# Optimization experiments

Measured on AMD Instinct MI355X. Metric: run time of the kernel, lower is better.

Reference implementation:

```python
import jax, jax.numpy as jnp
import numpy as np

C = 0.1          # curvature
EPS = 1e-8
BN_EPS = 1e-5
MAX_NORM = 0.9

def batchnorm_train(x, gamma, beta):
    mu = jnp.mean(x, axis=0)
    var = jnp.var(x, axis=0)  # biased, matches torch BN normalization
    return gamma * (x - mu) * jax.lax.rsqrt(var + BN_EPS) + beta

def euclidean_to_poincare(x, c=C, max_norm=MAX_NORM):
    norm = jnp.linalg.norm(x, axis=-1, keepdims=True)
    zeros_mask = norm == 0
    safe_norm = jnp.where(zeros_mask, jnp.ones_like(norm), norm)
    sqrt_c = jnp.sqrt(jnp.asarray(c, x.dtype))
    scale = max_norm * jnp.tanh(sqrt_c * norm) / (sqrt_c * safe_norm)
    return jnp.where(zeros_mask, jnp.zeros_like(x), scale * x)

def poincare_to_euclidean(x, c=C):
    norms = jnp.linalg.norm(x, axis=-1, keepdims=True)
    norms = jnp.clip(norms, 1e-8, 1.0 - 1e-8)
    sqrt_c = jnp.sqrt(jnp.asarray(c, x.dtype))
    return x * jnp.arctanh(sqrt_c * norms) / (sqrt_c * norms)

def batch_poincare_exp_map(x, v, c=C):
    x_nsq = jnp.sum(x * x, axis=-1, keepdims=True)
    lambda_x = 2.0 / (1.0 - c * x_nsq + EPS)
    v_norm = jnp.linalg.norm(v, axis=-1, keepdims=True)
    v_norm = jnp.maximum(v_norm, EPS)
    sqrt_c = jnp.sqrt(jnp.asarray(c, x.dtype))
    scale = jnp.tanh(sqrt_c * lambda_x * v_norm / 2.0) / (sqrt_c * v_norm)
    sv = scale * v
    numerator = (1.0 - c * x_nsq) * sv
    x_sv = jnp.sum(x * sv, axis=-1, keepdims=True)
    sv_nsq = jnp.sum(sv * sv, axis=-1, keepdims=True)
    denom = 1.0 - 2.0 * c * x_sv + c * c * x_nsq * sv_nsq
    result = x + numerator / (denom + EPS)
    mask = jnp.all(jnp.isfinite(result), axis=-1, keepdims=True)
    return jnp.where(mask, result, jnp.zeros_like(result))

def batch_poincare_log_map(x, y, c=C):
    x_nsq = jnp.sum(x * x, axis=-1, keepdims=True)
    lambda_x = 2.0 / (1.0 - c * x_nsq + EPS)
    y_nsq = jnp.sum(y * y, axis=-1, keepdims=True)
    xy = jnp.sum(x * y, axis=-1, keepdims=True)
    numerator = (1.0 - 2.0 * c * xy + c * y_nsq) * x - (1.0 - c * x_nsq) * y
    denom = 1.0 - 2.0 * c * xy + c * c * x_nsq * y_nsq
    diff = numerator / (denom + EPS)
    diff_norm = jnp.linalg.norm(diff, axis=-1, keepdims=True)
    diff_norm = jnp.maximum(diff_norm, EPS)
    sqrt_c = jnp.sqrt(jnp.asarray(c, x.dtype))
    return 2.0 / (sqrt_c * lambda_x) * jnp.arctanh(sqrt_c * diff_norm) * diff / diff_norm

def setup_inputs() -> dict:
    key = jax.random.key(0)
    ks = jax.random.split(key, 8)
    B, D_IN, H, D_OUT = 8192, 1024, 2048, 1000
    x = jax.random.normal(ks[0], (B, D_IN), dtype=jnp.float32)
    # kaiming_normal fan_out: std = sqrt(2/fan_out) with fan_out = out_features
    W1 = jax.random.normal(ks[1], (H, D_IN), dtype=jnp.float32) * np.sqrt(2.0 / H)
    b1 = jnp.zeros((H,), jnp.float32)
    g1 = jnp.ones((H,), jnp.float32)
    be1 = jnp.zeros((H,), jnp.float32)
    W2 = jax.random.normal(ks[2], (H, H), dtype=jnp.float32) * np.sqrt(2.0 / H)
    b2 = jnp.zeros((H,), jnp.float32)
    g2 = jnp.ones((H,), jnp.float32)
    be2 = jnp.zeros((H,), jnp.float32)
    W3 = jax.random.normal(ks[3], (D_OUT, H), dtype=jnp.float32) * np.sqrt(2.0 / D_OUT)
    b3 = jnp.zeros((D_OUT,), jnp.float32)
    return {"x": x, "W1": W1, "b1": b1, "g1": g1, "be1": be1,
            "W2": W2, "b2": b2, "g2": g2, "be2": be2, "W3": W3, "b3": b3}

def reference(x, W1, b1, g1, be1, W2, b2, g2, be2, W3, b3):
    h1 = jax.nn.relu(batchnorm_train(x @ W1.T + b1, g1, be1))
    h1_hyp = euclidean_to_poincare(h1)
    origin = jnp.zeros_like(h1_hyp)
    h1_tan = batch_poincare_log_map(origin, h1_hyp)
    h2_tan = jax.nn.relu(batchnorm_train(h1_tan @ W2.T + b2, g2, be2))
    h2_hyp = batch_poincare_exp_map(origin, h2_tan)
    h2_euc = poincare_to_euclidean(h2_hyp)
    out = h2_euc @ W3.T + b3
    return jax.nn.log_softmax(out, axis=1)
```

## Files before the change

kernel.cpp:

```cpp
#include <hip/hip_runtime.h>

typedef __bf16 bf16x8 __attribute__((ext_vector_type(8)));
typedef float f32x16 __attribute__((ext_vector_type(16)));
typedef unsigned short us8 __attribute__((ext_vector_type(8)));

#define AS1 __attribute__((address_space(1)))
#define AS3 __attribute__((address_space(3)))

__device__ __forceinline__ unsigned short f2bf(float x) {
  unsigned int u = __float_as_uint(x);
  u += 0x7fffu + ((u >> 16) & 1u);
  return (unsigned short)(u >> 16);
}
__device__ __forceinline__ float bf2f(unsigned short u) {
  return __uint_as_float(((unsigned int)u) << 16);
}
__device__ __forceinline__ void async_copy16(const void* g, void* l) {
  __builtin_amdgcn_global_load_lds((AS1 void*)(g), (AS3 void*)(l), 16, 0, 0);
}

__global__ void __launch_bounds__(256) k_prep(const float* __restrict__ x,
                                              const float* __restrict__ W1,
                                              const float* __restrict__ W2,
                                              const float* __restrict__ W3,
                                              unsigned short* __restrict__ Xb,
                                              unsigned short* __restrict__ W1b,
                                              unsigned short* __restrict__ W2b,
                                              unsigned short* __restrict__ W3b,
                                              float* __restrict__ P) {
  const long n1 = 2097152, n2 = 524288, n3 = 1048576, n4 = 524288;
  long i = (long)blockIdx.x * 256 + threadIdx.x;
  const float* s = nullptr;
  unsigned short* d = nullptr;
  long j = i;
  if (i < n1)                { s = x;  d = Xb; }
  else if ((j -= n1) < n2)   { s = W1; d = W1b; }
  else if ((j -= n2) < n3)   { s = W2; d = W2b; }
  else if ((j -= n3) < n4) {
    ushort4 o;
    if ((j >> 9) < 1000) {
      float4 v = ((const float4*)W3)[j];
      o.x = f2bf(v.x); o.y = f2bf(v.y); o.z = f2bf(v.z); o.w = f2bf(v.w);
    } else { o.x = 0; o.y = 0; o.z = 0; o.w = 0; }
    ((ushort4*)W3b)[j] = o;
    return;
  } else {
    j -= n4;
    ((float4*)P)[j] = (float4){0.f, 0.f, 0.f, 0.f};
    return;
  }
  float4 v = ((const float4*)s)[j];
  ushort4 o;
  o.x = f2bf(v.x); o.y = f2bf(v.y); o.z = f2bf(v.z); o.w = f2bf(v.w);
  ((ushort4*)d)[j] = o;
}

template <bool OUTBF16, bool STATS>
__global__ void __launch_bounds__(256, 2) k_gemm(const unsigned short* __restrict__ A,
                                                 const unsigned short* __restrict__ B,
                                                 void* __restrict__ Cout,
                                                 void* __restrict__ Cout2, int K,
                                                 int lda, int ldb, int ldc,
                                                 float* __restrict__ P) {
  __shared__ __align__(16) unsigned short lA[128 * 64];
  __shared__ __align__(16) unsigned short lB[256 * 64];
  const int tid = threadIdx.x;
  const int wave = tid >> 6;
  const int lane = tid & 63;

  const int f = blockIdx.x + gridDim.x * blockIdx.y;
  const int xcd = f & 7;
  const int fi = f >> 3;
  const int nblk = fi % gridDim.x;
  const int mblk = fi / gridDim.x + (gridDim.y >> 3) * xcd;
  const long m0 = (long)mblk * 128;
  const long n0 = (long)nblk * 256;
  const long koff = (long)blockIdx.z * K;

  const int rsub = lane >> 3;
  const int qg = ((lane & 7) ^ rsub) * 8;
  const unsigned short* gA = A + (m0 + wave * 32 + rsub) * (long)lda + koff + qg;
  const unsigned short* gB = B + (n0 + wave * 64 + rsub) * (long)ldb + koff + qg;
  unsigned short* lAw = lA + (wave * 32) * 64;
  unsigned short* lBw = lB + (wave * 64) * 64;

  const int wr = (wave >> 1) * 64;
  const int wc = (wave & 1) * 128;
  const int l31 = lane & 31;
  const int khalf = lane >> 5;
  const int r7 = l31 & 7;

  f32x16 acc[2][4];
#pragma unroll
  for (int i = 0; i < 2; ++i)
#pragma unroll
    for (int j = 0; j < 4; ++j) acc[i][j] = (f32x16)(0.f);

  for (int k0 = 0; k0 < K; k0 += 64) {
#pragma unroll
    for (int r = 0; r < 4; ++r)
      async_copy16(gA + (long)(r * 8) * lda + k0, lAw + r * 8 * 64);
#pragma unroll
    for (int r = 0; r < 8; ++r)
      async_copy16(gB + (long)(r * 8) * ldb + k0, lBw + r * 8 * 64);
    __syncthreads();

#pragma unroll
    for (int ks = 0; ks < 4; ++ks) {
      const int off = ((ks * 2 + khalf) ^ r7) * 8;
      bf16x8 af[2], bfr[4];
#pragma unroll
      for (int i = 0; i < 2; ++i)
        af[i] = *(const bf16x8*)&lA[(wr + i * 32 + l31) * 64 + off];
#pragma unroll
      for (int j = 0; j < 4; ++j)
        bfr[j] = *(const bf16x8*)&lB[(wc + j * 32 + l31) * 64 + off];
#pragma unroll
      for (int i = 0; i < 2; ++i)
#pragma unroll
        for (int j = 0; j < 4; ++j)
          acc[i][j] = __builtin_amdgcn_mfma_f32_32x32x16_bf16(af[i], bfr[j], acc[i][j], 0, 0, 0);
    }
    __syncthreads();
  }

  const int rbase = 4 * khalf;
  if (OUTBF16) {
    unsigned short* C = (unsigned short*)(blockIdx.z ? Cout2 : Cout);
#pragma unroll
    for (int i = 0; i < 2; ++i)
#pragma unroll
      for (int j = 0; j < 4; ++j) {
        long col = n0 + wc + j * 32 + l31;
#pragma unroll
        for (int reg = 0; reg < 16; ++reg) {
          long row = m0 + wr + i * 32 + (reg & 3) + 8 * (reg >> 2) + rbase;
          C[row * (long)ldc + col] = f2bf(acc[i][j][reg]);
        }
      }
  } else {
    float* C = (float*)(blockIdx.z ? Cout2 : Cout);
#pragma unroll
    for (int i = 0; i < 2; ++i)
#pragma unroll
      for (int j = 0; j < 4; ++j) {
        long col = n0 + wc + j * 32 + l31;
#pragma unroll
        for (int reg = 0; reg < 16; ++reg) {
          long row = m0 + wr + i * 32 + (reg & 3) + 8 * (reg >> 2) + rbase;
          C[row * (long)ldc + col] = acc[i][j][reg];
        }
      }
  }

  if (STATS) {
    float* sred = (float*)lA;
    sred[tid] = 0.f;
    sred[256 + tid] = 0.f;
    __syncthreads();
#pragma unroll
    for (int j = 0; j < 4; ++j) {
      float s = 0.f, s2 = 0.f;
#pragma unroll
      for (int i = 0; i < 2; ++i)
#pragma unroll
        for (int reg = 0; reg < 16; ++reg) {
          float v = acc[i][j][reg];
          s += v;
          s2 = fmaf(v, v, s2);
        }
      int cl = wc + j * 32 + l31;
      atomicAdd(&sred[cl], s);
      atomicAdd(&sred[256 + cl], s2);
    }
    __syncthreads();
    atomicAdd(&P[n0 + tid], sred[tid]);
    atomicAdd(&P[2048 + n0 + tid], sred[256 + tid]);
  }
}

template <bool STAGE2>
__global__ void __launch_bounds__(256) k_fuse(const unsigned short* __restrict__ Zb,
                                              const float* __restrict__ P,
                                              const float* __restrict__ g,
                                              const float* __restrict__ be,
                                              unsigned short* __restrict__ Ab) {
  const int t = threadIdx.x, wave = t >> 6, lane = t & 63;
  const long row = (long)blockIdx.x * 4 + wave;

  float sc[32], sh[32];
#pragma unroll
  for (int c = 0; c < 4; ++c) {
    int b4 = (lane + 64 * c) * 2;
    float4 s0 = ((const float4*)P)[b4],       s1 = ((const float4*)P)[b4 + 1];
    float4 q0 = ((const float4*)P)[512 + b4], q1 = ((const float4*)P)[512 + b4 + 1];
    float4 g0 = ((const float4*)g)[b4],       g1 = ((const float4*)g)[b4 + 1];
    float4 e0 = ((const float4*)be)[b4],      e1 = ((const float4*)be)[b4 + 1];
    float sm[8] = {s0.x, s0.y, s0.z, s0.w, s1.x, s1.y, s1.z, s1.w};
    float sq[8] = {q0.x, q0.y, q0.z, q0.w, q1.x, q1.y, q1.z, q1.w};
    float gg[8] = {g0.x, g0.y, g0.z, g0.w, g1.x, g1.y, g1.z, g1.w};
    float bb[8] = {e0.x, e0.y, e0.z, e0.w, e1.x, e1.y, e1.z, e1.w};
#pragma unroll
    for (int j = 0; j < 8; ++j) {
      float mean = sm[j] * (1.f / 8192.f);
      float var = sq[j] * (1.f / 8192.f) - mean * mean;
      float a = gg[j] * rsqrtf(var + 1e-5f);
      sc[c * 8 + j] = a;
      sh[c * 8 + j] = bb[j] - mean * a;
    }
  }

  const us8* zr = (const us8*)(Zb + row * 2048);
  float v[32];
  float ss = 0.f;
#pragma unroll
  for (int c = 0; c < 4; ++c) {
    us8 z8 = zr[lane + 64 * c];
#pragma unroll
    for (int j = 0; j < 8; ++j) {
      float xv = fmaxf(fmaf(bf2f(z8[j]), sc[c * 8 + j], sh[c * 8 + j]), 0.f);
      v[c * 8 + j] = xv;
      ss = fmaf(xv, xv, ss);
    }
  }
#pragma unroll
  for (int o = 32; o > 0; o >>= 1) ss += __shfl_xor(ss, o, 64);
  float n2 = ss;

  const float rsc = 0.31622776601683794f;
  float fac;
  if (STAGE2) {
    float nn = sqrtf(n2);
    float vn = fmaxf(nn, 1e-8f);
    float tt = rsc * vn;
    float scl = tanhf(tt) / tt;
    float hn = scl * nn;
    float cn = fminf(fmaxf(hn, 1e-8f), 1.0f);
    float z = rsc * cn;
    fac = scl * (atanhf(z) / z);
  } else {
    fac = 0.f;
    if (n2 > 0.f) {
      float n = sqrtf(n2);
      float th = tanhf(rsc * n);
      float s = 0.9f * th / (rsc * n);
      float dn = fmaxf(s * n, 1e-8f);
      float z = rsc * dn;
      fac = -(atanhf(z) / z) * s;
    }
  }
  us8* dr = (us8*)(Ab + row * 2048);
#pragma unroll
  for (int c = 0; c < 4; ++c) {
    us8 o8;
#pragma unroll
    for (int j = 0; j < 8; ++j) o8[j] = f2bf(v[c * 8 + j] * fac);
    dr[lane + 64 * c] = o8;
  }
}

__global__ void __launch_bounds__(256) k_lsm(const unsigned short* __restrict__ Za,
                                             const unsigned short* __restrict__ Zb2,
                                             const float* __restrict__ b3,
                                             float* __restrict__ out) {
  const int t = threadIdx.x, wave = t >> 6, lane = t & 63;
  const long row = (long)blockIdx.x * 4 + wave;
  const unsigned short* za = Za + row * 1024;
  const unsigned short* zb = Zb2 + row * 1024;
  float v[16];
  float mx = -3.4e38f;
#pragma unroll
  for (int c = 0; c < 16; ++c) {
    int col = lane + 64 * c;
    if (col < 1000) {
      v[c] = bf2f(za[col]) + bf2f(zb[col]) + b3[col];
      mx = fmaxf(mx, v[c]);
    } else v[c] = -3.4e38f;
  }
#pragma unroll
  for (int o = 32; o > 0; o >>= 1) mx = fmaxf(mx, __shfl_xor(mx, o, 64));

  float se = 0.f;
#pragma unroll
  for (int c = 0; c < 16; ++c) {
    int col = lane + 64 * c;
    if (col < 1000) se += expf(v[c] - mx);
  }
#pragma unroll
  for (int o = 32; o > 0; o >>= 1) se += __shfl_xor(se, o, 64);
  float ls = logf(se);

  float* orow = out + row * 1000;
#pragma unroll
  for (int c = 0; c < 16; ++c) {
    int col = lane + 64 * c;
    if (col < 1000) orow[col] = v[c] - mx - ls;
  }
}

extern "C" void kernel_launch(void* const* d_in, const int* in_sizes, int n_in,
                              void* d_out, int out_size, void* d_ws, size_t ws_size,
                              hipStream_t stream) {
  (void)in_sizes; (void)n_in; (void)out_size; (void)ws_size;
  const float* x   = (const float*)d_in[0];
  const float* W1  = (const float*)d_in[1];
  const float* g1  = (const float*)d_in[3];
  const float* be1 = (const float*)d_in[4];
  const float* W2  = (const float*)d_in[5];
  const float* g2  = (const float*)d_in[7];
  const float* be2 = (const float*)d_in[8];
  const float* W3  = (const float*)d_in[9];
  const float* b3  = (const float*)d_in[10];
  float* out = (float*)d_out;

  char* ws = (char*)d_ws;
  size_t off = 0;
  auto alloc = [&](size_t bytes) {
    void* p = ws + off;
    off += (bytes + 255) & ~(size_t)255;
    return p;
  };
  unsigned short* Xb  = (unsigned short*)alloc((size_t)8192 * 1024 * 2);
  unsigned short* W1b = (unsigned short*)alloc((size_t)2048 * 1024 * 2);
  unsigned short* W2b = (unsigned short*)alloc((size_t)2048 * 2048 * 2);
  unsigned short* W3b = (unsigned short*)alloc((size_t)1024 * 2048 * 2);
  unsigned short* Zb  = (unsigned short*)alloc((size_t)8192 * 2048 * 2);
  unsigned short* Ab  = (unsigned short*)alloc((size_t)8192 * 2048 * 2);
  unsigned short* Z3a = (unsigned short*)alloc((size_t)8192 * 1024 * 2);
  float* P            = (float*)alloc((size_t)2 * 4096 * 4);
  float* P2 = P + 4096;
  unsigned short* Z3b = Zb;

  k_prep<<<16392, 256, 0, stream>>>(x, W1, W2, W3, Xb, W1b, W2b, W3b, P);

  k_gemm<true, true><<<dim3(8, 64, 1), 256, 0, stream>>>(Xb, W1b, Zb, Zb, 1024, 1024, 1024, 2048, P);
  k_fuse<false><<<2048, 256, 0, stream>>>(Zb, P, g1, be1, Ab);

  k_gemm<true, true><<<dim3(8, 64, 1), 256, 0, stream>>>(Ab, W2b, Zb, Zb, 2048, 2048, 2048, 2048, P2);
  k_fuse<true><<<2048, 256, 0, stream>>>(Zb, P2, g2, be2, Ab);

  k_gemm<true, false><<<dim3(4, 64, 2), 256, 0, stream>>>(Ab, W3b, Z3a, Z3b, 1024, 2048, 2048, 1024, nullptr);
  k_lsm<<<2048, 256, 0, stream>>>(Z3a, Z3b, b3, out);
}
```

Baseline: 317.5 us.

## Double-buffer GEMM LDS tiles with 8-wave 256x256 blocks and phased async loads

Rewrites the bf16 MFMA GEMM to use 256x256 output tiles with 512 threads (8 waves) and double-buffered LDS. Each K step is split into four phases, and each phase issues part of the next tile's global-to-LDS async copies while MFMAs run on the current buffer. Raw s_barrier/vmcnt waits and s_setprio replace the __syncthreads pairs. The goal is to hide memory latency and raise data reuse per block. In exchange it uses 128KB of LDS, launches half as many blocks, and depends on hand-tuned waitcnt ordering being correct.

```diff
diff --git a/kernel.cpp b/kernel.cpp
--- a/kernel.cpp
+++ b/kernel.cpp
@@ -18,6 +18,9 @@
 __device__ __forceinline__ void async_copy16(const void* g, void* l) {
   __builtin_amdgcn_global_load_lds((AS1 void*)(g), (AS3 void*)(l), 16, 0, 0);
 }
+
+#define BARRIER() asm volatile("s_barrier" ::: "memory")
+#define WAITV(n) asm volatile("s_waitcnt vmcnt(" #n ")" ::: "memory")
 
 __global__ void __launch_bounds__(256) k_prep(const float* __restrict__ x,
                                               const float* __restrict__ W1,
@@ -56,126 +59,207 @@
 }
 
 template <bool OUTBF16, bool STATS>
-__global__ void __launch_bounds__(256, 2) k_gemm(const unsigned short* __restrict__ A,
+__global__ void __launch_bounds__(512, 2) k_gemm(const unsigned short* __restrict__ A,
                                                  const unsigned short* __restrict__ B,
                                                  void* __restrict__ Cout,
                                                  void* __restrict__ Cout2, int K,
                                                  int lda, int ldb, int ldc,
                                                  float* __restrict__ P) {
-  __shared__ __align__(16) unsigned short lA[128 * 64];
-  __shared__ __align__(16) unsigned short lB[256 * 64];
+  __shared__ __align__(16) unsigned short lA[2][256 * 64];
+  __shared__ __align__(16) unsigned short lB[2][256 * 64];
   const int tid = threadIdx.x;
   const int wave = tid >> 6;
   const int lane = tid & 63;
+  const int l31 = lane & 31;
+  const int khi = lane >> 5;
+  const int r7 = l31 & 7;
+  const int wrh = wave >> 2;
+  const int wcn = wave & 3;
 
   const int f = blockIdx.x + gridDim.x * blockIdx.y;
   const int xcd = f & 7;
   const int fi = f >> 3;
   const int nblk = fi % gridDim.x;
   const int mblk = fi / gridDim.x + (gridDim.y >> 3) * xcd;
-  const long m0 = (long)mblk * 128;
+  const long m0 = (long)mblk * 256;
   const long n0 = (long)nblk * 256;
   const long koff = (long)blockIdx.z * K;
+  const int NT = K >> 6;
 
   const int rsub = lane >> 3;
   const int qg = ((lane & 7) ^ rsub) * 8;
-  const unsigned short* gA = A + (m0 + wave * 32 + rsub) * (long)lda + koff + qg;
-  const unsigned short* gB = B + (n0 + wave * 64 + rsub) * (long)ldb + koff + qg;
-  unsigned short* lAw = lA + (wave * 32) * 64;
-  unsigned short* lBw = lB + (wave * 64) * 64;
-
-  const int wr = (wave >> 1) * 64;
-  const int wc = (wave & 1) * 128;
-  const int l31 = lane & 31;
-  const int khalf = lane >> 5;
-  const int r7 = l31 & 7;
-
-  f32x16 acc[2][4];
-#pragma unroll
-  for (int i = 0; i < 2; ++i)
-#pragma unroll
-    for (int j = 0; j < 4; ++j) acc[i][j] = (f32x16)(0.f);
-
-  for (int k0 = 0; k0 < K; k0 += 64) {
-#pragma unroll
-    for (int r = 0; r < 4; ++r)
-      async_copy16(gA + (long)(r * 8) * lda + k0, lAw + r * 8 * 64);
-#pragma unroll
-    for (int r = 0; r < 8; ++r)
-      async_copy16(gB + (long)(r * 8) * ldb + k0, lBw + r * 8 * 64);
-    __syncthreads();
-
-#pragma unroll
-    for (int ks = 0; ks < 4; ++ks) {
-      const int off = ((ks * 2 + khalf) ^ r7) * 8;
-      bf16x8 af[2], bfr[4];
-#pragma unroll
-      for (int i = 0; i < 2; ++i)
-        af[i] = *(const bf16x8*)&lA[(wr + i * 32 + l31) * 64 + off];
-#pragma unroll
-      for (int j = 0; j < 4; ++j)
-        bfr[j] = *(const bf16x8*)&lB[(wc + j * 32 + l31) * 64 + off];
-#pragma unroll
-      for (int i = 0; i < 2; ++i)
-#pragma unroll
-        for (int j = 0; j < 4; ++j)
-          acc[i][j] = __builtin_amdgcn_mfma_f32_32x32x16_bf16(af[i], bfr[j], acc[i][j], 0, 0, 0);
-    }
-    __syncthreads();
-  }
-
-  const int rbase = 4 * khalf;
+  const unsigned short* gAq0 = A + (m0 +       8 * wave + rsub) * (long)lda + koff + qg;
+  const unsigned short* gAq1 = A + (m0 +  64 + 8 * wave + rsub) * (long)lda + koff + qg;
+  const unsigned short* gAq2 = A + (m0 + 128 + 8 * wave + rsub) * (long)lda + koff + qg;
+  const unsigned short* gAq3 = A + (m0 + 192 + 8 * wave + rsub) * (long)lda + koff + qg;
+  const unsigned short* gB0  = B + (n0 + 32 * wave + rsub) * (long)ldb + koff + qg;
+  const unsigned short* gB1  = gB0 +  8 * (long)ldb;
+  const unsigned short* gB2  = gB0 + 16 * (long)ldb;
+  const unsigned short* gB3  = gB0 + 24 * (long)ldb;
+  const int dAq0 = (      8 * wave) * 64;
+  const int dAq1 = ( 64 + 8 * wave) * 64;
+  const int dAq2 = (128 + 8 * wave) * 64;
+  const int dAq3 = (192 + 8 * wave) * 64;
+  const int dB0  = (32 * wave) * 64;
+
+  f32x16 acc[4][2];
+#pragma unroll
+  for (int i = 0; i < 4; ++i)
+#pragma unroll
+    for (int j = 0; j < 2; ++j) acc[i][j] = (f32x16)(0.f);
+
+#define PH_READS(rh, kh, DOB)                                                        \
+  bf16x8 af[2][2];                                                                   \
+  _Pragma("unroll") for (int i = 0; i < 2; ++i) {                                    \
+    _Pragma("unroll") for (int ks = 0; ks < 2; ++ks) {                               \
+      af[i][ks] = *(const bf16x8*)&lAc[(wrh * 128 + (rh) * 64 + i * 32 + l31) * 64 + \
+                                       ((((kh) * 2 + ks) * 2 + khi) ^ r7) * 8];      \
+    }                                                                                \
+  }                                                                                  \
+  if (DOB) {                                                                         \
+    _Pragma("unroll") for (int j = 0; j < 2; ++j) {                                  \
+      _Pragma("unroll") for (int ks = 0; ks < 2; ++ks) {                             \
+        bf[j][ks] = *(const bf16x8*)&lBc[(wcn * 64 + j * 32 + l31) * 64 +            \
+                                         ((((kh) * 2 + ks) * 2 + khi) ^ r7) * 8];    \
+      }                                                                              \
+    }                                                                                \
+  }
+
+#define PH_MFMA(rh)                                                                 \
+  __builtin_amdgcn_s_setprio(1);                                                    \
+  _Pragma("unroll") for (int ks = 0; ks < 2; ++ks) {                                 \
+    _Pragma("unroll") for (int i = 0; i < 2; ++i) {                                  \
+      _Pragma("unroll") for (int j = 0; j < 2; ++j) {                                \
+        acc[(rh) * 2 + i][j] = __builtin_amdgcn_mfma_f32_32x32x16_bf16(              \
+            af[i][ks], bf[j][ks], acc[(rh) * 2 + i][j], 0, 0, 0);                    \
+      }                                                                              \
+    }                                                                                \
+  }                                                                                  \
+  __builtin_amdgcn_s_setprio(0);
+
+  {
+    unsigned short* lAn = &lA[0][0];
+    unsigned short* lBn = &lB[0][0];
+    async_copy16(gAq0, lAn + dAq0);
+    async_copy16(gAq2, lAn + dAq2);
+    async_copy16(gB0,  lBn + dB0);
+    async_copy16(gB1,  lBn + dB0 + 8 * 64);
+    async_copy16(gB2,  lBn + dB0 + 16 * 64);
+    async_copy16(gB3,  lBn + dB0 + 24 * 64);
+    async_copy16(gAq1, lAn + dAq1);
+    async_copy16(gAq3, lAn + dAq3);
+    WAITV(2);
+    BARRIER();
+  }
+
+  for (int t = 0; t < NT - 1; ++t) {
+    const unsigned short* lAc = &lA[t & 1][0];
+    const unsigned short* lBc = &lB[t & 1][0];
+    unsigned short* lAn = &lA[(t + 1) & 1][0];
+    unsigned short* lBn = &lB[(t + 1) & 1][0];
+    const long kk = (long)(t + 1) * 64;
+    bf16x8 bf[2][2];
+    {
+      PH_READS(0, 0, 1)
+      async_copy16(gAq0 + kk, lAn + dAq0);
+      async_copy16(gAq2 + kk, lAn + dAq2);
+      BARRIER();
+      PH_MFMA(0)
+      WAITV(2);
+      BARRIER();
+    }
+    {
+      PH_READS(1, 0, 0)
+      async_copy16(gB0 + kk, lBn + dB0);
+      async_copy16(gB1 + kk, lBn + dB0 + 8 * 64);
+      BARRIER();
+      PH_MFMA(1)
+      BARRIER();
+    }
+    {
+      PH_READS(0, 1, 1)
+      async_copy16(gB2 + kk, lBn + dB0 + 16 * 64);
+      async_copy16(gB3 + kk, lBn + dB0 + 24 * 64);
+      BARRIER();
+      PH_MFMA(0)
+      BARRIER();
+    }
+    {
+      PH_READS(1, 1, 0)
+      async_copy16(gAq1 + kk, lAn + dAq1);
+      async_copy16(gAq3 + kk, lAn + dAq3);
+      BARRIER();
+      PH_MFMA(1)
+      WAITV(2);
+      BARRIER();
+    }
+  }
+
+  {
+    const unsigned short* lAc = &lA[(NT - 1) & 1][0];
+    const unsigned short* lBc = &lB[(NT - 1) & 1][0];
+    bf16x8 bf[2][2];
+    { PH_READS(0, 0, 1) BARRIER(); PH_MFMA(0) WAITV(0); BARRIER(); }
+    { PH_READS(1, 0, 0) BARRIER(); PH_MFMA(1) BARRIER(); }
+    { PH_READS(0, 1, 1) BARRIER(); PH_MFMA(0) BARRIER(); }
+    { PH_READS(1, 1, 0) BARRIER(); PH_MFMA(1) BARRIER(); }
+  }
+#undef PH_READS
+#undef PH_MFMA
+
+  const int rbase = 4 * khi;
+  const long crow0 = m0 + wrh * 128;
+  const long ccol0 = n0 + wcn * 64;
   if (OUTBF16) {
     unsigned short* C = (unsigned short*)(blockIdx.z ? Cout2 : Cout);
 #pragma unroll
-    for (int i = 0; i < 2; ++i)
-#pragma unroll
-      for (int j = 0; j < 4; ++j) {
-        long col = n0 + wc + j * 32 + l31;
+    for (int ig = 0; ig < 4; ++ig)
+#pragma unroll
+      for (int j = 0; j < 2; ++j) {
+        long col = ccol0 + j * 32 + l31;
 #pragma unroll
         for (int reg = 0; reg < 16; ++reg) {
-          long row = m0 + wr + i * 32 + (reg & 3) + 8 * (reg >> 2) + rbase;
-          C[row * (long)ldc + col] = f2bf(acc[i][j][reg]);
+          long row = crow0 + ig * 32 + (reg & 3) + 8 * (reg >> 2) + rbase;
+          C[row * (long)ldc + col] = f2bf(acc[ig][j][reg]);
         }
       }
   } else {
     float* C = (float*)(blockIdx.z ? Cout2 : Cout);
 #pragma unroll
-    for (int i = 0; i < 2; ++i)
-#pragma unroll
-      for (int j = 0; j < 4; ++j) {
-        long col = n0 + wc + j * 32 + l31;
+    for (int ig = 0; ig < 4; ++ig)
+#pragma unroll
+      for (int j = 0; j < 2; ++j) {
+        long col = ccol0 + j * 32 + l31;
 #pragma unroll
         for (int reg = 0; reg < 16; ++reg) {
-          long row = m0 + wr + i * 32 + (reg & 3) + 8 * (reg >> 2) + rbase;
-          C[row * (long)ldc + col] = acc[i][j][reg];
+          long row = crow0 + ig * 32 + (reg & 3) + 8 * (reg >> 2) + rbase;
+          C[row * (long)ldc + col] = acc[ig][j][reg];
         }
       }
   }
 
   if (STATS) {
-    float* sred = (float*)lA;
+    float* sred = (float*)&lA[0][0];
     sred[tid] = 0.f;
-    sred[256 + tid] = 0.f;
     __syncthreads();
 #pragma unroll
-    for (int j = 0; j < 4; ++j) {
+    for (int j = 0; j < 2; ++j) {
       float s = 0.f, s2 = 0.f;
 #pragma unroll
-      for (int i = 0; i < 2; ++i)
+      for (int ig = 0; ig < 4; ++ig)
 #pragma unroll
         for (int reg = 0; reg < 16; ++reg) {
-          float v = acc[i][j][reg];
+          float v = acc[ig][j][reg];
           s += v;
           s2 = fmaf(v, v, s2);
         }
-      int cl = wc + j * 32 + l31;
+      int cl = wcn * 64 + j * 32 + l31;
       atomicAdd(&sred[cl], s);
       atomicAdd(&sred[256 + cl], s2);
     }
     __syncthreads();
-    atomicAdd(&P[n0 + tid], sred[tid]);
-    atomicAdd(&P[2048 + n0 + tid], sred[256 + tid]);
+    if (tid < 256) atomicAdd(&P[n0 + tid], sred[tid]);
+    else           atomicAdd(&P[2048 + n0 + tid - 256], sred[tid]);
   }
 }
 
@@ -333,12 +417,12 @@
 
   k_prep<<<16392, 256, 0, stream>>>(x, W1, W2, W3, Xb, W1b, W2b, W3b, P);
 
-  k_gemm<true, true><<<dim3(8, 64, 1), 256, 0, stream>>>(Xb, W1b, Zb, Zb, 1024, 1024, 1024, 2048, P);
+  k_gemm<true, true><<<dim3(8, 32, 1), 512, 0, stream>>>(Xb, W1b, Zb, Zb, 1024, 1024, 1024, 2048, P);
   k_fuse<false><<<2048, 256, 0, stream>>>(Zb, P, g1, be1, Ab);
 
-  k_gemm<true, true><<<dim3(8, 64, 1), 256, 0, stream>>>(Ab, W2b, Zb, Zb, 2048, 2048, 2048, 2048, P2);
+  k_gemm<true, true><<<dim3(8, 32, 1), 512, 0, stream>>>(Ab, W2b, Zb, Zb, 2048, 2048, 2048, 2048, P2);
   k_fuse<true><<<2048, 256, 0, stream>>>(Zb, P2, g2, be2, Ab);
 
-  k_gemm<true, false><<<dim3(4, 64, 2), 256, 0, stream>>>(Ab, W3b, Z3a, Z3b, 1024, 2048, 2048, 1024, nullptr);
+  k_gemm<true, false><<<dim3(4, 32, 2), 512, 0, stream>>>(Ab, W3b, Z3a, Z3b, 1024, 2048, 2048, 1024, nullptr);
   k_lsm<<<2048, 256, 0, stream>>>(Z3a, Z3b, b3, out);
 }
```

After: 317.6 us. About the same (+0.0%).

## Enlarge GEMM tile to 256x256 and double-buffer LDS with async prefetch

Applied to the files above, without the earlier changes.

The GEMM block tile grows from 128x256 to 256x256, giving each wave a 128x128 sub-tile with 4x4 MFMA accumulators. LDS is double-buffered so the next K-slice is fetched with global_load_lds while the current one is computed, using explicit vmcnt waits and s_barrier in place of two __syncthreads per iteration. The aim is more operand reuse per byte loaded and overlap of memory with MFMA work. In exchange, occupancy drops to one block per CU with 128KB of LDS and many more accumulator registers, and the grid is halved, which may leave CUs idle.

```diff
diff --git a/kernel.cpp b/kernel.cpp
--- a/kernel.cpp
+++ b/kernel.cpp
@@ -18,6 +18,9 @@
 __device__ __forceinline__ void async_copy16(const void* g, void* l) {
   __builtin_amdgcn_global_load_lds((AS1 void*)(g), (AS3 void*)(l), 16, 0, 0);
 }
+
+#define BARRIER() asm volatile("s_barrier" ::: "memory")
+#define WAITV(n) asm volatile("s_waitcnt vmcnt(" #n ")" ::: "memory")
 
 __global__ void __launch_bounds__(256) k_prep(const float* __restrict__ x,
                                               const float* __restrict__ W1,
@@ -56,120 +59,132 @@
 }
 
 template <bool OUTBF16, bool STATS>
-__global__ void __launch_bounds__(256, 2) k_gemm(const unsigned short* __restrict__ A,
+__global__ void __launch_bounds__(256, 1) k_gemm(const unsigned short* __restrict__ A,
                                                  const unsigned short* __restrict__ B,
                                                  void* __restrict__ Cout,
                                                  void* __restrict__ Cout2, int K,
                                                  int lda, int ldb, int ldc,
                                                  float* __restrict__ P) {
-  __shared__ __align__(16) unsigned short lA[128 * 64];
-  __shared__ __align__(16) unsigned short lB[256 * 64];
+  __shared__ __align__(16) unsigned short lA[2][256 * 64];
+  __shared__ __align__(16) unsigned short lB[2][256 * 64];
   const int tid = threadIdx.x;
   const int wave = tid >> 6;
   const int lane = tid & 63;
+  const int l31 = lane & 31;
+  const int khi = lane >> 5;
+  const int r7 = l31 & 7;
+  const int wrh = wave >> 1;
+  const int wcn = wave & 1;
 
   const int f = blockIdx.x + gridDim.x * blockIdx.y;
   const int xcd = f & 7;
   const int fi = f >> 3;
   const int nblk = fi % gridDim.x;
   const int mblk = fi / gridDim.x + (gridDim.y >> 3) * xcd;
-  const long m0 = (long)mblk * 128;
+  const long m0 = (long)mblk * 256;
   const long n0 = (long)nblk * 256;
   const long koff = (long)blockIdx.z * K;
+  const int NT = K >> 6;
 
   const int rsub = lane >> 3;
   const int qg = ((lane & 7) ^ rsub) * 8;
-  const unsigned short* gA = A + (m0 + wave * 32 + rsub) * (long)lda + koff + qg;
-  const unsigned short* gB = B + (n0 + wave * 64 + rsub) * (long)ldb + koff + qg;
-  unsigned short* lAw = lA + (wave * 32) * 64;
-  unsigned short* lBw = lB + (wave * 64) * 64;
-
-  const int wr = (wave >> 1) * 64;
-  const int wc = (wave & 1) * 128;
-  const int l31 = lane & 31;
-  const int khalf = lane >> 5;
-  const int r7 = l31 & 7;
-
-  f32x16 acc[2][4];
-#pragma unroll
-  for (int i = 0; i < 2; ++i)
+  const long lda8 = (long)lda * 8;
+  const long ldb8 = (long)ldb * 8;
+  const unsigned short* gAw = A + (m0 + wave * 64 + rsub) * (long)lda + koff + qg;
+  const unsigned short* gBw = B + (n0 + wave * 64 + rsub) * (long)ldb + koff + qg;
+  const int dW = (wave * 64) * 64;
+
+  f32x16 acc[4][4];
+#pragma unroll
+  for (int i = 0; i < 4; ++i)
 #pragma unroll
     for (int j = 0; j < 4; ++j) acc[i][j] = (f32x16)(0.f);
 
-  for (int k0 = 0; k0 < K; k0 += 64) {
-#pragma unroll
-    for (int r = 0; r < 4; ++r)
-      async_copy16(gA + (long)(r * 8) * lda + k0, lAw + r * 8 * 64);
-#pragma unroll
-    for (int r = 0; r < 8; ++r)
-      async_copy16(gB + (long)(r * 8) * ldb + k0, lBw + r * 8 * 64);
-    __syncthreads();
-
+  auto stage = [&](int buf, long kk) {
+    unsigned short* dA = &lA[buf][0] + dW;
+    unsigned short* dB = &lB[buf][0] + dW;
+#pragma unroll
+    for (int i = 0; i < 8; ++i)
+      async_copy16(gAw + (long)i * lda8 + kk, dA + i * 8 * 64);
+#pragma unroll
+    for (int i = 0; i < 8; ++i)
+      async_copy16(gBw + (long)i * ldb8 + kk, dB + i * 8 * 64);
+  };
+
+  stage(0, 0);
+  for (int t = 0; t < NT; ++t) {
+    const unsigned short* lAc = &lA[t & 1][0];
+    const unsigned short* lBc = &lB[t & 1][0];
+    WAITV(0);
+    BARRIER();
+    if (t + 1 < NT) stage((t + 1) & 1, (long)(t + 1) * 64);
 #pragma unroll
     for (int ks = 0; ks < 4; ++ks) {
-      const int off = ((ks * 2 + khalf) ^ r7) * 8;
-      bf16x8 af[2], bfr[4];
-#pragma unroll
-      for (int i = 0; i < 2; ++i)
-        af[i] = *(const bf16x8*)&lA[(wr + i * 32 + l31) * 64 + off];
-#pragma unroll
-      for (int j = 0; j < 4; ++j)
-        bfr[j] = *(const bf16x8*)&lB[(wc + j * 32 + l31) * 64 + off];
-#pragma unroll
-      for (int i = 0; i < 2; ++i)
-#pragma unroll
-        for (int j = 0; j < 4; ++j)
-          acc[i][j] = __builtin_amdgcn_mfma_f32_32x32x16_bf16(af[i], bfr[j], acc[i][j], 0, 0, 0);
-    }
-    __syncthreads();
-  }
-
-  const int rbase = 4 * khalf;
+      const int off = ((ks * 2 + khi) ^ r7) * 8;
+      bf16x8 af[4], bfr[4];
+#pragma unroll
+      for (int m = 0; m < 4; ++m)
+        af[m] = *(const bf16x8*)&lAc[(wrh * 128 + m * 32 + l31) * 64 + off];
+#pragma unroll
+      for (int n = 0; n < 4; ++n)
+        bfr[n] = *(const bf16x8*)&lBc[(wcn * 128 + n * 32 + l31) * 64 + off];
+#pragma unroll
+      for (int m = 0; m < 4; ++m)
+#pragma unroll
+        for (int n = 0; n < 4; ++n)
+          acc[m][n] = __builtin_amdgcn_mfma_f32_32x32x16_bf16(af[m], bfr[n], acc[m][n], 0, 0, 0);
+    }
+  }
+
+  const int rbase = 4 * khi;
+  const long crow0 = m0 + wrh * 128;
+  const long ccol0 = n0 + wcn * 128;
   if (OUTBF16) {
     unsigned short* C = (unsigned short*)(blockIdx.z ? Cout2 : Cout);
 #pragma unroll
-    for (int i = 0; i < 2; ++i)
-#pragma unroll
-      for (int j = 0; j < 4; ++j) {
-        long col = n0 + wc + j * 32 + l31;
+    for (int m = 0; m < 4; ++m)
+#pragma unroll
+      for (int n = 0; n < 4; ++n) {
+        long col = ccol0 + n * 32 + l31;
 #pragma unroll
         for (int reg = 0; reg < 16; ++reg) {
-          long row = m0 + wr + i * 32 + (reg & 3) + 8 * (reg >> 2) + rbase;
-          C[row * (long)ldc + col] = f2bf(acc[i][j][reg]);
+          long row = crow0 + m * 32 + (reg & 3) + 8 * (reg >> 2) + rbase;
+          C[row * (long)ldc + col] = f2bf(acc[m][n][reg]);
         }
       }
   } else {
     float* C = (float*)(blockIdx.z ? Cout2 : Cout);
 #pragma unroll
-    for (int i = 0; i < 2; ++i)
-#pragma unroll
-      for (int j = 0; j < 4; ++j) {
-        long col = n0 + wc + j * 32 + l31;
+    for (int m = 0; m < 4; ++m)
+#pragma unroll
+      for (int n = 0; n < 4; ++n) {
+        long col = ccol0 + n * 32 + l31;
 #pragma unroll
         for (int reg = 0; reg < 16; ++reg) {
-          long row = m0 + wr + i * 32 + (reg & 3) + 8 * (reg >> 2) + rbase;
-          C[row * (long)ldc + col] = acc[i][j][reg];
+          long row = crow0 + m * 32 + (reg & 3) + 8 * (reg >> 2) + rbase;
+          C[row * (long)ldc + col] = acc[m][n][reg];
         }
       }
   }
 
   if (STATS) {
-    float* sred = (float*)lA;
+    float* sred = (float*)&lA[0][0];
+    __syncthreads();
     sred[tid] = 0.f;
     sred[256 + tid] = 0.f;
     __syncthreads();
 #pragma unroll
-    for (int j = 0; j < 4; ++j) {
+    for (int n = 0; n < 4; ++n) {
       float s = 0.f, s2 = 0.f;
 #pragma unroll
-      for (int i = 0; i < 2; ++i)
+      for (int m = 0; m < 4; ++m)
 #pragma unroll
         for (int reg = 0; reg < 16; ++reg) {
-          float v = acc[i][j][reg];
+          float v = acc[m][n][reg];
           s += v;
           s2 = fmaf(v, v, s2);
         }
-      int cl = wc + j * 32 + l31;
+      int cl = wcn * 128 + n * 32 + l31;
       atomicAdd(&sred[cl], s);
       atomicAdd(&sred[256 + cl], s2);
     }
@@ -333,12 +348,12 @@
 
   k_prep<<<16392, 256, 0, stream>>>(x, W1, W2, W3, Xb, W1b, W2b, W3b, P);
 
-  k_gemm<true, true><<<dim3(8, 64, 1), 256, 0, stream>>>(Xb, W1b, Zb, Zb, 1024, 1024, 1024, 2048, P);
+  k_gemm<true, true><<<dim3(8, 32, 1), 256, 0, stream>>>(Xb, W1b, Zb, Zb, 1024, 1024, 1024, 2048, P);
   k_fuse<false><<<2048, 256, 0, stream>>>(Zb, P, g1, be1, Ab);
 
-  k_gemm<true, true><<<dim3(8, 64, 1), 256, 0, stream>>>(Ab, W2b, Zb, Zb, 2048, 2048, 2048, 2048, P2);
+  k_gemm<true, true><<<dim3(8, 32, 1), 256, 0, stream>>>(Ab, W2b, Zb, Zb, 2048, 2048, 2048, 2048, P2);
   k_fuse<true><<<2048, 256, 0, stream>>>(Zb, P2, g2, be2, Ab);
 
-  k_gemm<true, false><<<dim3(4, 64, 2), 256, 0, stream>>>(Ab, W3b, Z3a, Z3b, 1024, 2048, 2048, 1024, nullptr);
+  k_gemm<true, false><<<dim3(4, 32, 2), 256, 0, stream>>>(Ab, W3b, Z3a, Z3b, 1024, 2048, 2048, 1024, nullptr);
   k_lsm<<<2048, 256, 0, stream>>>(Z3a, Z3b, b3, out);
 }
```

New measurement: 336.3 us. +5.9%, slower.
